# Performance work log

Measured on AMD Instinct MI355X. Metric: run time of the kernel, lower is better.

Reference implementation:

```python
import jax, jax.numpy as jnp
import numpy as np

B = 4096      # batch
D = 256       # flattened input feature dim
NUMFEAT = 1 + D + D * (D + 1) // 2  # 33153: bias + linear + quadratic terms


def setup_inputs() -> dict:
    key = jax.random.key(0)
    k1, k2 = jax.random.split(key)
    x = jax.random.normal(k1, (B, D), dtype=jnp.float32)
    # nn.Linear(numfeat, 10, bias=False): weight shape (10, numfeat)
    W = jax.random.normal(k2, (10, NUMFEAT), dtype=jnp.float32) * 0.01
    return {"x": x, "W": W}


def reference(x, W):
    # x: (B, D) -- original does x.view(B, -1); already 2D here.
    b, d = x.shape
    # sklearn PolynomialFeatures(degree=2) column order:
    # [1, x_0..x_{d-1}, x_0*x_0, x_0*x_1, ..., x_{d-1}*x_{d-1}]
    # i.e. combinations_with_replacement == upper-triangular (incl. diagonal)
    iu0, iu1 = np.triu_indices(d)  # static index constants
    ones = jnp.ones((b, 1), dtype=x.dtype)
    cross = x[:, iu0] * x[:, iu1]          # (B, D*(D+1)/2)
    feats = jnp.concatenate([ones, x, cross], axis=1)  # (B, NUMFEAT)
    return feats @ W.T                      # (B, 10)
```

## Files before the change

kernel.cpp:

```cpp
#include <hip/hip_runtime.h>


#define DD 256
#define NF 33153
#define TPB 256
#define ASTRIDE 264

typedef __attribute__((ext_vector_type(8))) short short8;
typedef __attribute__((ext_vector_type(4))) float floatx4;
typedef __attribute__((ext_vector_type(4), aligned(4))) float float4a;

union S8U { unsigned u[4]; short8 s; };

__device__ inline unsigned pack2(float lo, float hi) {
    unsigned a = __builtin_bit_cast(unsigned, hi) + 0x8000u;
    unsigned b = __builtin_bit_cast(unsigned, lo) + 0x8000u;
    return __builtin_amdgcn_perm(a, b, 0x07060302u);
}

__global__ __launch_bounds__(TPB)
void gbuild_kernel(const float* __restrict__ W, unsigned short* __restrict__ G) {
    int oi = blockIdx.x * 8 + (threadIdx.x >> 5);
    int c0 = (threadIdx.x & 31) * 8;
    int o = oi >> 8, i = oi & 255;
    int base = o * NF + 257 + i * 255 - ((i * (i - 1)) >> 1);
    float4a w0 = *(const float4a*)&W[base + c0];
    float4a w1 = *(const float4a*)&W[base + c0 + 4];
    float f[8] = {w0.x, w0.y, w0.z, w0.w, w1.x, w1.y, w1.z, w1.w};
#pragma unroll
    for (int e = 0; e < 8; ++e)
        if (c0 + e < i) f[e] = 0.f;
    S8U p;
    p.u[0] = pack2(f[0], f[1]); p.u[1] = pack2(f[2], f[3]);
    p.u[2] = pack2(f[4], f[5]); p.u[3] = pack2(f[6], f[7]);
    *(short8*)&G[oi * DD + c0] = p.s;
}

__global__ __launch_bounds__(TPB, 3)
void PolynomialRegression_75385265979710_kernel(const float* __restrict__ x,
                                                const float* __restrict__ W,
                                                const unsigned short* __restrict__ G,
                                                float* __restrict__ out) {
    __shared__ __align__(16) unsigned short As[64 * ASTRIDE];
    __shared__ float red[4 * 64];

    const int tid  = threadIdx.x;
    const int lane = tid & 63, wave = tid >> 6;
    const int ln   = lane & 15, quad = lane >> 4;
    const int q8   = quad * 8;
    const int rowbase = blockIdx.x * 64;
    const int o  = blockIdx.y;
    const int g1 = wave, g2 = 7 - wave;
    const int rem = 8 - wave;

#pragma unroll
    for (int it = 0; it < 8; ++it) {
        int idx = it * 2048 + tid * 8;
        int r = idx >> 8, c = idx & 255;
        const float* src = &x[(rowbase + r) * DD + c];
        float4a v0 = *(const float4a*)src;
        float4a v1 = *(const float4a*)(src + 4);
        S8U p;
        p.u[0] = pack2(v0.x, v0.y); p.u[1] = pack2(v0.z, v0.w);
        p.u[2] = pack2(v1.x, v1.y); p.u[3] = pack2(v1.z, v1.w);
        *(short8*)&As[r * ASTRIDE + c] = p.s;
    }

    int iRow[4];
    float w1v[4];
#pragma unroll
    for (int nt = 0; nt < 4; ++nt) {
        int g = (nt < 2) ? g1 : g2;
        iRow[nt] = g * 32 + (nt & 1) * 16 + ln;
        w1v[nt]  = W[o * NF + 1 + iRow[nt]];
    }
    const float bias = W[o * NF];

    __syncthreads();

    floatx4 acc[4][4];
#pragma unroll
    for (int mt = 0; mt < 4; ++mt)
#pragma unroll
        for (int nt = 0; nt < 4; ++nt) acc[mt][nt] = (floatx4)0.f;

    const unsigned short* Gy = G + (o * DD) * DD;

#pragma unroll
    for (int t = 0; t < 9; ++t) {
        const bool first = (t < rem);
        const int g  = first ? g1 : g2;
        const int kc = first ? (g1 + t) : (g2 + (t - rem));
        const unsigned short* gb = Gy + (g * 32 + ln) * DD + kc * 32 + q8;
        short8 b0 = *(const short8*)gb;
        short8 b1 = *(const short8*)(gb + 16 * DD);
        short8 a[4];
#pragma unroll
        for (int mt = 0; mt < 4; ++mt)
            a[mt] = *(const short8*)&As[(mt * 16 + ln) * ASTRIDE + kc * 32 + q8];
        if (first) {
#pragma unroll
            for (int mt = 0; mt < 4; ++mt) {
                acc[mt][0] = __builtin_amdgcn_mfma_f32_16x16x32_bf16(a[mt], b0, acc[mt][0], 0, 0, 0);
                acc[mt][1] = __builtin_amdgcn_mfma_f32_16x16x32_bf16(a[mt], b1, acc[mt][1], 0, 0, 0);
            }
        } else {
#pragma unroll
            for (int mt = 0; mt < 4; ++mt) {
                acc[mt][2] = __builtin_amdgcn_mfma_f32_16x16x32_bf16(a[mt], b0, acc[mt][2], 0, 0, 0);
                acc[mt][3] = __builtin_amdgcn_mfma_f32_16x16x32_bf16(a[mt], b1, acc[mt][3], 0, 0, 0);
            }
        }
    }

#pragma unroll
    for (int mt = 0; mt < 4; ++mt) {
#pragma unroll
        for (int r = 0; r < 4; ++r) {
            const int m = mt * 16 + quad * 4 + r;
            float p = 0.f;
#pragma unroll
            for (int nt = 0; nt < 4; ++nt) {
                unsigned u = As[m * ASTRIDE + iRow[nt]];
                float xv = __builtin_bit_cast(float, u << 16);
                p = fmaf(xv, acc[mt][nt][r] + w1v[nt], p);
            }
            p += __shfl_xor(p, 1);
            p += __shfl_xor(p, 2);
            p += __shfl_xor(p, 4);
            p += __shfl_xor(p, 8);
            if (ln == 0) red[wave * 64 + m] = p;
        }
    }
    __syncthreads();

    if (tid < 64) {
        float s = red[tid] + red[64 + tid] + red[128 + tid] + red[192 + tid]
                + bias;
        out[(rowbase + tid) * 10 + o] = s;
    }
}

extern "C" void kernel_launch(void* const* d_in, const int* in_sizes, int n_in,
                              void* d_out, int out_size, void* d_ws, size_t ws_size,
                              hipStream_t stream) {
    const float* x = (const float*)d_in[0];
    const float* W = (const float*)d_in[1];
    float* out = (float*)d_out;

    unsigned short* G = (unsigned short*)d_ws;

    gbuild_kernel<<<2560 / 8, TPB, 0, stream>>>(W, G);

    dim3 grid(4096 / 64, 10);
    PolynomialRegression_75385265979710_kernel<<<grid, TPB, 0, stream>>>(x, W, G, out);
}
```

Baseline: 69.17 us.

## Fuse weight-matrix bf16 packing into main kernel, drop gbuild pre-pass

Removes the separate kernel that rebuilt the upper-triangular weight matrix as a dense bf16 buffer. The main kernel now reads fp32 weights straight from W using computed triangular row offsets, masks the lower-triangle entries on the diagonal tiles, and packs them to bf16 in registers before the MFMA. This saves a kernel launch and a global round-trip through the workspace. In exchange, every block reads twice as many bytes of weights, repeats the pack work across 64 row blocks, and the loads are unaligned fp32 ones.

```diff
diff --git a/kernel.cpp b/kernel.cpp
--- a/kernel.cpp
+++ b/kernel.cpp
@@ -18,28 +18,9 @@
     return __builtin_amdgcn_perm(a, b, 0x07060302u);
 }
 
-__global__ __launch_bounds__(TPB)
-void gbuild_kernel(const float* __restrict__ W, unsigned short* __restrict__ G) {
-    int oi = blockIdx.x * 8 + (threadIdx.x >> 5);
-    int c0 = (threadIdx.x & 31) * 8;
-    int o = oi >> 8, i = oi & 255;
-    int base = o * NF + 257 + i * 255 - ((i * (i - 1)) >> 1);
-    float4a w0 = *(const float4a*)&W[base + c0];
-    float4a w1 = *(const float4a*)&W[base + c0 + 4];
-    float f[8] = {w0.x, w0.y, w0.z, w0.w, w1.x, w1.y, w1.z, w1.w};
-#pragma unroll
-    for (int e = 0; e < 8; ++e)
-        if (c0 + e < i) f[e] = 0.f;
-    S8U p;
-    p.u[0] = pack2(f[0], f[1]); p.u[1] = pack2(f[2], f[3]);
-    p.u[2] = pack2(f[4], f[5]); p.u[3] = pack2(f[6], f[7]);
-    *(short8*)&G[oi * DD + c0] = p.s;
-}
-
 __global__ __launch_bounds__(TPB, 3)
 void PolynomialRegression_75385265979710_kernel(const float* __restrict__ x,
                                                 const float* __restrict__ W,
-                                                const unsigned short* __restrict__ G,
                                                 float* __restrict__ out) {
     __shared__ __align__(16) unsigned short As[64 * ASTRIDE];
     __shared__ float red[4 * 64];
@@ -76,6 +57,15 @@
     }
     const float bias = W[o * NF];
 
+    int rb[2][2];
+#pragma unroll
+    for (int gg = 0; gg < 2; ++gg) {
+        int g = gg ? g2 : g1;
+        int i0 = g * 32 + ln, i1 = i0 + 16;
+        rb[gg][0] = o * NF + 257 + i0 * 255 - ((i0 * (i0 - 1)) >> 1) + q8;
+        rb[gg][1] = o * NF + 257 + i1 * 255 - ((i1 * (i1 - 1)) >> 1) + q8;
+    }
+
     __syncthreads();
 
     floatx4 acc[4][4];
@@ -84,20 +74,38 @@
 #pragma unroll
         for (int nt = 0; nt < 4; ++nt) acc[mt][nt] = (floatx4)0.f;
 
-    const unsigned short* Gy = G + (o * DD) * DD;
-
 #pragma unroll
     for (int t = 0; t < 9; ++t) {
-        const bool first = (t < rem);
-        const int g  = first ? g1 : g2;
-        const int kc = first ? (g1 + t) : (g2 + (t - rem));
-        const unsigned short* gb = Gy + (g * 32 + ln) * DD + kc * 32 + q8;
-        short8 b0 = *(const short8*)gb;
-        short8 b1 = *(const short8*)(gb + 16 * DD);
+        const bool first  = (t < rem);
+        const int  gg     = first ? 0 : 1;
+        const int  kc     = first ? (g1 + t) : (g2 + (t - rem));
+        const bool masked = (t == 0) || (t == rem);
+
+        const float* p0 = &W[rb[gg][0] + kc * 32];
+        const float* p1 = &W[rb[gg][1] + kc * 32];
+        float4a w00 = *(const float4a*)p0, w01 = *(const float4a*)(p0 + 4);
+        float4a w10 = *(const float4a*)p1, w11 = *(const float4a*)(p1 + 4);
+        float f0[8] = {w00.x, w00.y, w00.z, w00.w, w01.x, w01.y, w01.z, w01.w};
+        float f1[8] = {w10.x, w10.y, w10.z, w10.w, w11.x, w11.y, w11.z, w11.w};
+        if (masked) {
+#pragma unroll
+            for (int e = 0; e < 8; ++e) {
+                if (q8 + e < ln)      f0[e] = 0.f;
+                if (q8 + e < ln + 16) f1[e] = 0.f;
+            }
+        }
+        S8U pb0, pb1;
+        pb0.u[0] = pack2(f0[0], f0[1]); pb0.u[1] = pack2(f0[2], f0[3]);
+        pb0.u[2] = pack2(f0[4], f0[5]); pb0.u[3] = pack2(f0[6], f0[7]);
+        pb1.u[0] = pack2(f1[0], f1[1]); pb1.u[1] = pack2(f1[2], f1[3]);
+        pb1.u[2] = pack2(f1[4], f1[5]); pb1.u[3] = pack2(f1[6], f1[7]);
+        short8 b0 = pb0.s, b1 = pb1.s;
+
         short8 a[4];
 #pragma unroll
         for (int mt = 0; mt < 4; ++mt)
             a[mt] = *(const short8*)&As[(mt * 16 + ln) * ASTRIDE + kc * 32 + q8];
+
         if (first) {
 #pragma unroll
             for (int mt = 0; mt < 4; ++mt) {
@@ -148,10 +156,6 @@
     const float* W = (const float*)d_in[1];
     float* out = (float*)d_out;
 
-    unsigned short* G = (unsigned short*)d_ws;
-
-    gbuild_kernel<<<2560 / 8, TPB, 0, stream>>>(W, G);
-
     dim3 grid(4096 / 64, 10);
-    PolynomialRegression_75385265979710_kernel<<<grid, TPB, 0, stream>>>(x, W, G, out);
+    PolynomialRegression_75385265979710_kernel<<<grid, TPB, 0, stream>>>(x, W, out);
 }
```

Measured after the change: 70.61 us. 1.02x slower.
